# Kernel tuning notes

Hardware: AMD Instinct MI355X
Metric: run time of the kernel (lower is better)

## Reference

```python
import jax, jax.numpy as jnp
import numpy as np

B, C, H, W = 8, 512, 32, 32
NUM_HEADS = 8
HEAD_DIM = C // NUM_HEADS


def setup_inputs() -> dict:
    key = jax.random.key(0)
    k1, k2, k3 = jax.random.split(key, 3)
    query = jax.random.normal(k1, (B, C, H, W), dtype=jnp.float32)
    key_value = jax.random.normal(k2, (B, C, H, W), dtype=jnp.float32)
    # Linear(dim, 3*dim): store as [C, 3C] so y = x @ W + b
    W_qkv = jax.random.normal(k3, (C, 3 * C), dtype=jnp.float32) * (C ** -0.5)
    b_qkv = jnp.zeros((3 * C,), dtype=jnp.float32)
    return {"query": query, "key_value": key_value, "W_qkv": W_qkv, "b_qkv": b_qkv}


def reference(query, key_value, W_qkv, b_qkv):
    Bb, Cc, Hh, Ww = query.shape
    seq = Hh * Ww
    scale = HEAD_DIM ** -0.5

    # [B, C, H, W] -> [B, S, C]
    q_seq = query.reshape(Bb, Cc, seq).transpose(0, 2, 1)
    kv_seq = key_value.reshape(Bb, Cc, seq).transpose(0, 2, 1)

    # Original calls full qkv_proj and slices; math == projecting with sliced weights.
    q = q_seq @ W_qkv[:, :Cc] + b_qkv[:Cc]
    k = kv_seq @ W_qkv[:, Cc:2 * Cc] + b_qkv[Cc:2 * Cc]
    v = kv_seq @ W_qkv[:, 2 * Cc:] + b_qkv[2 * Cc:]

    def heads(x):  # [B, S, C] -> [B, nH, S, hd]
        return x.reshape(Bb, seq, NUM_HEADS, HEAD_DIM).transpose(0, 2, 1, 3)

    q, k, v = heads(q), heads(k), heads(v)
    attn = jnp.einsum('bhqd,bhkd->bhqk', q, k) * scale
    attn = jax.nn.softmax(attn, axis=-1)  # dropout: identity in eval
    out = jnp.einsum('bhqk,bhkd->bhqd', attn, v)
    # [B, nH, S, hd] -> [B, S, C] -> [B, C, H, W]
    out = out.transpose(0, 2, 1, 3).reshape(Bb, seq, Cc)
    return out.transpose(0, 2, 1).reshape(Bb, Cc, Hh, Ww)
```

## Files before the change

kernel.cpp:

```cpp
#include <hip/hip_runtime.h>
#include <hip/hip_bf16.h>

using short4v = __attribute__((ext_vector_type(4))) short;
using short8  = __attribute__((ext_vector_type(8))) short;
using uint2v  = __attribute__((ext_vector_type(2))) unsigned int;
using f32x4   = __attribute__((ext_vector_type(4))) float;

static constexpr int CDIM = 512;
static constexpr float KSCALE = 0.125f * 1.44269504088896341f;

__device__ __forceinline__ short f2bf(float f) {
  unsigned u = __builtin_bit_cast(unsigned, f);
  u = (u + 0x7fffu + ((u >> 16) & 1u)) >> 16;
  return (short)(unsigned short)u;
}
__device__ __forceinline__ unsigned pack_bf16(float a, float b) {
  return (unsigned)(unsigned short)f2bf(a) | ((unsigned)(unsigned short)f2bf(b) << 16);
}

#define GLOAD_LDS16(gp, lp)                                                              \
  __builtin_amdgcn_global_load_lds((const __attribute__((address_space(1))) void*)(gp),  \
                                   (__attribute__((address_space(3))) void*)(lp), 16, 0, 0)
#define MFMA16(a, b, c) __builtin_amdgcn_mfma_f32_16x16x32_bf16((a), (b), (c), 0, 0, 0)
#define WAIT_LGKM0() __builtin_amdgcn_s_waitcnt(0xc07f)

__global__ __launch_bounds__(256) void prep_transpose(const float* __restrict__ query,
                                                      const float* __restrict__ keyv,
                                                      const float* __restrict__ Wqkv,
                                                      short* __restrict__ Xq_t,
                                                      short* __restrict__ Xkv_t,
                                                      short* __restrict__ W_t) {
  __shared__ float tile[64 * 65];
  const int id = blockIdx.x;
  const float* s; short* d; int R, C, r0, c0;
  if (id < 2048) {
    const int which = id >> 10;
    int rem = id & 1023;
    const int b = rem >> 7; rem &= 127;
    R = 512; C = 1024;
    s = (which ? keyv : query) + (size_t)b * 512 * 1024;
    d = (which ? Xkv_t : Xq_t) + (size_t)b * 512 * 1024;
    r0 = (rem >> 4) * 64; c0 = (rem & 15) * 64;
  } else {
    const int rem = id - 2048;
    R = 512; C = 1536; s = Wqkv; d = W_t;
    r0 = (rem / 24) * 64; c0 = (rem % 24) * 64;
  }
  const int t  = threadIdx.x;
  const int rr = t >> 4;
  const int c4 = (t & 15) * 4;
#pragma unroll
  for (int i = 0; i < 4; ++i) {
    const int r = rr + i * 16;
    f32x4 v = *(const f32x4*)(s + (size_t)(r0 + r) * C + c0 + c4);
#pragma unroll
    for (int j = 0; j < 4; ++j) tile[(c4 + j) * 65 + r] = v[j];
  }
  __syncthreads();
  const int r8 = (t & 7) * 8;
#pragma unroll
  for (int i = 0; i < 2; ++i) {
    const int c = (t >> 3) + i * 32;
    short8 pk;
#pragma unroll
    for (int j = 0; j < 8; ++j) pk[j] = f2bf(tile[c * 65 + r8 + j]);
    *(short8*)(d + (size_t)(c0 + c) * R + r0 + r8) = pk;
  }
}

__global__ __launch_bounds__(256, 3) void qkv_gemm(const short* __restrict__ Xq,
                                                   const short* __restrict__ Xkv,
                                                   const short* __restrict__ Wt,
                                                   const float* __restrict__ bias,
                                                   short* __restrict__ Qg,
                                                   short* __restrict__ Kg,
                                                   short* __restrict__ Vt) {
  __shared__ short Asm[128 * 64];
  __shared__ short Bsm[128 * 64];
  __shared__ short epi[4 * 1152];
  const int n0 = blockIdx.x * 128;
  const int m0 = blockIdx.y * 128;
  const short* A = (n0 < CDIM) ? Xq : Xkv;
  const int t = threadIdx.x;
  const int w = t >> 6, l = t & 63;
  const int wm = w & 1, wn = w >> 1;
  const int lc = l & 15, lr = l >> 4;

  f32x4 acc[4][4];
#pragma unroll
  for (int i = 0; i < 4; ++i)
#pragma unroll
    for (int j = 0; j < 4; ++j) acc[i][j] = (f32x4){0.f, 0.f, 0.f, 0.f};

  for (int kb = 0; kb < 8; ++kb) {
    const int k0 = kb * 64;
#pragma unroll
    for (int i = 0; i < 4; ++i) {
      const int Qi = (w * 4 + i) * 64 + l;
      const int m = Qi >> 3, kq = Qi & 7;
      GLOAD_LDS16(A  + (size_t)(m0 + m) * CDIM + k0 + kq * 8, &Asm[Qi * 8]);
      GLOAD_LDS16(Wt + (size_t)(n0 + m) * CDIM + k0 + kq * 8, &Bsm[Qi * 8]);
    }
    __syncthreads();
#pragma unroll
    for (int kc = 0; kc < 2; ++kc) {
      short8 af[4], bfr[4];
#pragma unroll
      for (int mt = 0; mt < 4; ++mt)
        af[mt] = *(const short8*)(&Asm[(wm * 64 + mt * 16 + lc) * 64 + kc * 32 + lr * 8]);
#pragma unroll
      for (int nt = 0; nt < 4; ++nt)
        bfr[nt] = *(const short8*)(&Bsm[(wn * 64 + nt * 16 + lc) * 64 + kc * 32 + lr * 8]);
#pragma unroll
      for (int mt = 0; mt < 4; ++mt)
#pragma unroll
        for (int nt = 0; nt < 4; ++nt)
          acc[mt][nt] = MFMA16(af[mt], bfr[nt], acc[mt][nt]);
    }
    __syncthreads();
  }

  const int N0 = n0 + wn * 64, M0 = m0 + wm * 64;
  const int hg = N0 >> 6;
  const int part = hg >> 3, hh = hg & 7;
  const int bb = M0 >> 10, s0 = M0 & 1023;
  float bv[4];
#pragma unroll
  for (int nt = 0; nt < 4; ++nt) bv[nt] = bias[N0 + nt * 16 + lc];
  short* slab = epi + w * 1152;

  if (part < 2) {
    const float osc = part ? 1.f : KSCALE;
    short* obase = (part ? Kg : Qg) + (size_t)(bb * 8 + hh) * 65536 + (size_t)s0 * 64;
#pragma unroll
    for (int mt = 0; mt < 4; ++mt) {
#pragma unroll
      for (int nt = 0; nt < 4; ++nt)
#pragma unroll
        for (int r = 0; r < 4; ++r)
          slab[(lr * 4 + r) * 72 + nt * 16 + lc] = f2bf((acc[mt][nt][r] + bv[nt]) * osc);
      WAIT_LGKM0();
#pragma unroll
      for (int i = 0; i < 2; ++i) {
        const int slot = i * 64 + l;
        const int m_l = slot >> 3, n8 = (slot & 7) * 8;
        short8 vv = *(const short8*)(&slab[m_l * 72 + n8]);
        *(short8*)(obase + (size_t)(mt * 16 + m_l) * 64 + n8) = vv;
      }
      WAIT_LGKM0();
    }
  } else {
    short* vbase = Vt + (size_t)(bb * 8 + hh) * 65536;
#pragma unroll
    for (int nt = 0; nt < 4; ++nt) {
#pragma unroll
      for (int mt = 0; mt < 4; ++mt)
#pragma unroll
        for (int r = 0; r < 4; ++r)
          slab[lc * 72 + mt * 16 + lr * 4 + r] = f2bf(acc[mt][nt][r] + bv[nt]);
      WAIT_LGKM0();
#pragma unroll
      for (int i = 0; i < 2; ++i) {
        const int slot = i * 64 + l;
        const int dloc = slot >> 3, ch = (slot & 7) * 8;
        short8 vv = *(const short8*)(&slab[dloc * 72 + ch]);
        *(short8*)(vbase + (size_t)(nt * 16 + dloc) * 1024 + s0 + ch) = vv;
      }
      WAIT_LGKM0();
    }
  }
}

__global__ __launch_bounds__(256, 2) void flash_attn(const short* __restrict__ Qg,
                                                     const short* __restrict__ Kg,
                                                     const short* __restrict__ Vt,
                                                     float* __restrict__ out) {
  __shared__ alignas(16) short smem[17408];
  short* Ksm = smem;
  short* Vsm = smem + 4096;
  const int b = blockIdx.z, h = blockIdx.y;
  const int q0 = blockIdx.x * 128;
  const int bh = b * 8 + h;
  const int t = threadIdx.x;
  const int w = t >> 6, l = t & 63;
  const int quad = l >> 4, l15 = l & 15;
  short* Pw = smem + 8192 + w * 2304;

  const short* Qbase = Qg + (size_t)bh * 65536;
  const short* Kbase = Kg + (size_t)bh * 65536;
  const short* Vbase = Vt + (size_t)bh * 65536;

  short8 bq[2][2];
#pragma unroll
  for (int qs = 0; qs < 2; ++qs) {
    const short* qrow = Qbase + (size_t)(q0 + qs * 64 + w * 16 + l15) * 64;
    bq[qs][0] = *(const short8*)(qrow + quad * 8);
    bq[qs][1] = *(const short8*)(qrow + 32 + quad * 8);
  }

  float lp[2] = {0.f, 0.f};
  f32x4 Oac[2][4];
#pragma unroll
  for (int qs = 0; qs < 2; ++qs)
#pragma unroll
    for (int dt = 0; dt < 4; ++dt) Oac[qs][dt] = (f32x4){0.f, 0.f, 0.f, 0.f};

  for (int it = 0; it < 16; ++it) {
    const int kk0 = it * 64;
#pragma unroll
    for (int i = 0; i < 2; ++i) {
      const int Qi = (w * 2 + i) * 64 + l;
      const int sr = Qi >> 3, u = Qi & 7;
      GLOAD_LDS16(Kbase + (size_t)(kk0 + sr) * 64 + (u ^ (sr & 7)) * 8, &Ksm[Qi * 8]);
      GLOAD_LDS16(Vbase + (size_t)sr * 1024 + kk0 + (u ^ (sr & 7)) * 8, &Vsm[Qi * 8]);
    }
    __syncthreads();

    short8 kf[2][4];
#pragma unroll
    for (int c = 0; c < 2; ++c)
#pragma unroll
      for (int nt = 0; nt < 4; ++nt) {
        const int srow = nt * 16 + l15;
        kf[c][nt] = *(const short8*)(&Ksm[(srow * 8 + ((c * 4 + quad) ^ (srow & 7))) * 8]);
      }

#pragma unroll
    for (int qs = 0; qs < 2; ++qs) {
      f32x4 st[4];
#pragma unroll
      for (int nt = 0; nt < 4; ++nt) {
        st[nt] = (f32x4){0.f, 0.f, 0.f, 0.f};
#pragma unroll
        for (int c = 0; c < 2; ++c) st[nt] = MFMA16(kf[c][nt], bq[qs][c], st[nt]);
      }
      short* Ps = Pw + qs * 1152;
#pragma unroll
      for (int nt = 0; nt < 4; ++nt) {
        float p0 = __builtin_amdgcn_exp2f(st[nt][0]);
        float p1 = __builtin_amdgcn_exp2f(st[nt][1]);
        float p2 = __builtin_amdgcn_exp2f(st[nt][2]);
        float p3 = __builtin_amdgcn_exp2f(st[nt][3]);
        lp[qs] += (p0 + p1) + (p2 + p3);
        uint2v pk;
        pk[0] = pack_bf16(p0, p1);
        pk[1] = pack_bf16(p2, p3);
        *(uint2v*)(&Ps[l15 * 72 + (nt * 4 + quad) * 4]) = pk;
      }
    }
    WAIT_LGKM0();

#pragma unroll
    for (int c = 0; c < 2; ++c) {
      short8 pb0 = *(const short8*)(&Pw[l15 * 72 + (c * 8 + quad * 2) * 4]);
      short8 pb1 = *(const short8*)(&Pw[1152 + l15 * 72 + (c * 8 + quad * 2) * 4]);
#pragma unroll
      for (int dt = 0; dt < 4; ++dt) {
        const int drow = dt * 16 + l15;
        short8 vf = *(const short8*)(&Vsm[(drow * 8 + ((c * 4 + quad) ^ (drow & 7))) * 8]);
        Oac[0][dt] = MFMA16(vf, pb0, Oac[0][dt]);
        Oac[1][dt] = MFMA16(vf, pb1, Oac[1][dt]);
      }
    }
    __syncthreads();
  }

#pragma unroll
  for (int qs = 0; qs < 2; ++qs) {
    float lv = lp[qs];
    lv += __shfl_xor(lv, 16, 64);
    lv += __shfl_xor(lv, 32, 64);
    const float rinv = 1.f / lv;
    float* ob = out + ((size_t)(b * 512 + h * 64)) * 1024 + q0 + qs * 64 + w * 16 + l15;
#pragma unroll
    for (int dt = 0; dt < 4; ++dt)
#pragma unroll
      for (int r = 0; r < 4; ++r)
        ob[(size_t)(dt * 16 + quad * 4 + r) * 1024] = Oac[qs][dt][r] * rinv;
  }
}

extern "C" void kernel_launch(void* const* d_in, const int* in_sizes, int n_in,
                              void* d_out, int out_size, void* d_ws, size_t ws_size,
                              hipStream_t stream) {
  const float* query = (const float*)d_in[0];
  const float* keyv  = (const float*)d_in[1];
  const float* Wqkv  = (const float*)d_in[2];
  const float* bqkv  = (const float*)d_in[3];
  float* out = (float*)d_out;
  short* ws  = (short*)d_ws;

  short* Xq_t  = ws;
  short* Xkv_t = ws + 4194304;
  short* W_t   = ws + 8388608;
  short* Qg    = ws + 9175040;
  short* Kg    = ws + 13369344;
  short* Vt    = ws + 17563648;

  prep_transpose<<<dim3(2240), 256, 0, stream>>>(query, keyv, Wqkv, Xq_t, Xkv_t, W_t);
  qkv_gemm<<<dim3(12, 64, 1), 256, 0, stream>>>(Xq_t, Xkv_t, W_t, bqkv, Qg, Kg, Vt);
  flash_attn<<<dim3(8, 8, 8), 256, 0, stream>>>(Qg, Kg, Vt, out);
}
```

Measured before the change: 136.9 us.

## Widen QKV GEMM tile to 128x256, swizzle LDS, reorder attention grid

The QKV projection GEMM tile grows from 128x128 to 128x256, giving each wave 4x8 accumulators and more MFMA work per A-fragment load. Both LDS tiles now use an XOR swizzle on 16-byte chunks to avoid bank conflicts on fragment reads. The epilogue loops over two heads per wave. The attention grid is reordered so batch*head is the fastest-varying block index, which changes the schedule and cache locality of K/V reuse. The costs are higher register pressure and occupancy lowered to 2 blocks per CU, and the GEMM grid drops to 384 blocks.

```diff
diff --git a/kernel.cpp b/kernel.cpp
--- a/kernel.cpp
+++ b/kernel.cpp
@@ -68,7 +68,7 @@
   }
 }
 
-__global__ __launch_bounds__(256, 3) void qkv_gemm(const short* __restrict__ Xq,
+__global__ __launch_bounds__(256, 2) void qkv_gemm(const short* __restrict__ Xq,
                                                    const short* __restrict__ Xkv,
                                                    const short* __restrict__ Wt,
                                                    const float* __restrict__ bias,
@@ -76,9 +76,9 @@
                                                    short* __restrict__ Kg,
                                                    short* __restrict__ Vt) {
   __shared__ short Asm[128 * 64];
-  __shared__ short Bsm[128 * 64];
+  __shared__ short Bsm[256 * 64];
   __shared__ short epi[4 * 1152];
-  const int n0 = blockIdx.x * 128;
+  const int n0 = blockIdx.x * 256;
   const int m0 = blockIdx.y * 128;
   const short* A = (n0 < CDIM) ? Xq : Xkv;
   const int t = threadIdx.x;
@@ -86,87 +86,102 @@
   const int wm = w & 1, wn = w >> 1;
   const int lc = l & 15, lr = l >> 4;
 
-  f32x4 acc[4][4];
+  f32x4 acc[4][8];
 #pragma unroll
   for (int i = 0; i < 4; ++i)
 #pragma unroll
-    for (int j = 0; j < 4; ++j) acc[i][j] = (f32x4){0.f, 0.f, 0.f, 0.f};
+    for (int j = 0; j < 8; ++j) acc[i][j] = (f32x4){0.f, 0.f, 0.f, 0.f};
 
   for (int kb = 0; kb < 8; ++kb) {
     const int k0 = kb * 64;
 #pragma unroll
     for (int i = 0; i < 4; ++i) {
       const int Qi = (w * 4 + i) * 64 + l;
-      const int m = Qi >> 3, kq = Qi & 7;
-      GLOAD_LDS16(A  + (size_t)(m0 + m) * CDIM + k0 + kq * 8, &Asm[Qi * 8]);
-      GLOAD_LDS16(Wt + (size_t)(n0 + m) * CDIM + k0 + kq * 8, &Bsm[Qi * 8]);
+      const int row = Qi >> 3, u = Qi & 7;
+      GLOAD_LDS16(A + (size_t)(m0 + row) * CDIM + k0 + ((u ^ (row & 7)) * 8), &Asm[Qi * 8]);
+    }
+#pragma unroll
+    for (int i = 0; i < 8; ++i) {
+      const int Qi = (w * 8 + i) * 64 + l;
+      const int row = Qi >> 3, u = Qi & 7;
+      GLOAD_LDS16(Wt + (size_t)(n0 + row) * CDIM + k0 + ((u ^ (row & 7)) * 8), &Bsm[Qi * 8]);
     }
     __syncthreads();
 #pragma unroll
     for (int kc = 0; kc < 2; ++kc) {
-      short8 af[4], bfr[4];
+      short8 af[4], bfr[8];
+#pragma unroll
+      for (int mt = 0; mt < 4; ++mt) {
+        const int row = wm * 64 + mt * 16 + lc;
+        af[mt] = *(const short8*)(&Asm[(row * 8 + ((kc * 4 + lr) ^ (row & 7))) * 8]);
+      }
+#pragma unroll
+      for (int nt = 0; nt < 8; ++nt) {
+        const int row = wn * 128 + nt * 16 + lc;
+        bfr[nt] = *(const short8*)(&Bsm[(row * 8 + ((kc * 4 + lr) ^ (row & 7))) * 8]);
+      }
 #pragma unroll
       for (int mt = 0; mt < 4; ++mt)
-        af[mt] = *(const short8*)(&Asm[(wm * 64 + mt * 16 + lc) * 64 + kc * 32 + lr * 8]);
-#pragma unroll
-      for (int nt = 0; nt < 4; ++nt)
-        bfr[nt] = *(const short8*)(&Bsm[(wn * 64 + nt * 16 + lc) * 64 + kc * 32 + lr * 8]);
-#pragma unroll
-      for (int mt = 0; mt < 4; ++mt)
-#pragma unroll
-        for (int nt = 0; nt < 4; ++nt)
+#pragma unroll
+        for (int nt = 0; nt < 8; ++nt)
           acc[mt][nt] = MFMA16(af[mt], bfr[nt], acc[mt][nt]);
     }
     __syncthreads();
   }
 
-  const int N0 = n0 + wn * 64, M0 = m0 + wm * 64;
-  const int hg = N0 >> 6;
-  const int part = hg >> 3, hh = hg & 7;
+  const int M0 = m0 + wm * 64;
   const int bb = M0 >> 10, s0 = M0 & 1023;
-  float bv[4];
-#pragma unroll
-  for (int nt = 0; nt < 4; ++nt) bv[nt] = bias[N0 + nt * 16 + lc];
+  const int N0 = n0 + wn * 128;
+  float bv[8];
+#pragma unroll
+  for (int nt = 0; nt < 8; ++nt) bv[nt] = bias[N0 + nt * 16 + lc];
   short* slab = epi + w * 1152;
 
-  if (part < 2) {
-    const float osc = part ? 1.f : KSCALE;
-    short* obase = (part ? Kg : Qg) + (size_t)(bb * 8 + hh) * 65536 + (size_t)s0 * 64;
-#pragma unroll
-    for (int mt = 0; mt < 4; ++mt) {
-#pragma unroll
-      for (int nt = 0; nt < 4; ++nt)
-#pragma unroll
-        for (int r = 0; r < 4; ++r)
-          slab[(lr * 4 + r) * 72 + nt * 16 + lc] = f2bf((acc[mt][nt][r] + bv[nt]) * osc);
-      WAIT_LGKM0();
-#pragma unroll
-      for (int i = 0; i < 2; ++i) {
-        const int slot = i * 64 + l;
-        const int m_l = slot >> 3, n8 = (slot & 7) * 8;
-        short8 vv = *(const short8*)(&slab[m_l * 72 + n8]);
-        *(short8*)(obase + (size_t)(mt * 16 + m_l) * 64 + n8) = vv;
-      }
-      WAIT_LGKM0();
-    }
-  } else {
-    short* vbase = Vt + (size_t)(bb * 8 + hh) * 65536;
-#pragma unroll
-    for (int nt = 0; nt < 4; ++nt) {
-#pragma unroll
-      for (int mt = 0; mt < 4; ++mt)
-#pragma unroll
-        for (int r = 0; r < 4; ++r)
-          slab[lc * 72 + mt * 16 + lr * 4 + r] = f2bf(acc[mt][nt][r] + bv[nt]);
-      WAIT_LGKM0();
-#pragma unroll
-      for (int i = 0; i < 2; ++i) {
-        const int slot = i * 64 + l;
-        const int dloc = slot >> 3, ch = (slot & 7) * 8;
-        short8 vv = *(const short8*)(&slab[dloc * 72 + ch]);
-        *(short8*)(vbase + (size_t)(nt * 16 + dloc) * 1024 + s0 + ch) = vv;
-      }
-      WAIT_LGKM0();
+#pragma unroll
+  for (int hi = 0; hi < 2; ++hi) {
+    const int hg = (N0 >> 6) + hi;
+    const int part = hg >> 3, hh = hg & 7;
+    const int nb = hi * 4;
+    if (part < 2) {
+      const float osc = part ? 1.f : KSCALE;
+      short* obase = (part ? Kg : Qg) + (size_t)(bb * 8 + hh) * 65536 + (size_t)s0 * 64;
+#pragma unroll
+      for (int mt = 0; mt < 4; ++mt) {
+#pragma unroll
+        for (int ntL = 0; ntL < 4; ++ntL)
+#pragma unroll
+          for (int r = 0; r < 4; ++r)
+            slab[(lr * 4 + r) * 72 + ntL * 16 + lc] =
+                f2bf((acc[mt][nb + ntL][r] + bv[nb + ntL]) * osc);
+        WAIT_LGKM0();
+#pragma unroll
+        for (int i = 0; i < 2; ++i) {
+          const int slot = i * 64 + l;
+          const int m_l = slot >> 3, n8 = (slot & 7) * 8;
+          short8 vv = *(const short8*)(&slab[m_l * 72 + n8]);
+          *(short8*)(obase + (size_t)(mt * 16 + m_l) * 64 + n8) = vv;
+        }
+        WAIT_LGKM0();
+      }
+    } else {
+      short* vbase = Vt + (size_t)(bb * 8 + hh) * 65536;
+#pragma unroll
+      for (int ntL = 0; ntL < 4; ++ntL) {
+#pragma unroll
+        for (int mt = 0; mt < 4; ++mt)
+#pragma unroll
+          for (int r = 0; r < 4; ++r)
+            slab[lc * 72 + mt * 16 + lr * 4 + r] = f2bf(acc[mt][nb + ntL][r] + bv[nb + ntL]);
+        WAIT_LGKM0();
+#pragma unroll
+        for (int i = 0; i < 2; ++i) {
+          const int slot = i * 64 + l;
+          const int dloc = slot >> 3, ch = (slot & 7) * 8;
+          short8 vv = *(const short8*)(&slab[dloc * 72 + ch]);
+          *(short8*)(vbase + (size_t)(ntL * 16 + dloc) * 1024 + s0 + ch) = vv;
+        }
+        WAIT_LGKM0();
+      }
     }
   }
 }
@@ -178,9 +193,9 @@
   __shared__ alignas(16) short smem[17408];
   short* Ksm = smem;
   short* Vsm = smem + 4096;
-  const int b = blockIdx.z, h = blockIdx.y;
-  const int q0 = blockIdx.x * 128;
-  const int bh = b * 8 + h;
+  const int bh = blockIdx.x;
+  const int b = bh >> 3, h = bh & 7;
+  const int q0 = blockIdx.y * 128;
   const int t = threadIdx.x;
   const int w = t >> 6, l = t & 63;
   const int quad = l >> 4, l15 = l & 15;
@@ -298,6 +313,6 @@
   short* Vt    = ws + 17563648;
 
   prep_transpose<<<dim3(2240), 256, 0, stream>>>(query, keyv, Wqkv, Xq_t, Xkv_t, W_t);
-  qkv_gemm<<<dim3(12, 64, 1), 256, 0, stream>>>(Xq_t, Xkv_t, W_t, bqkv, Qg, Kg, Vt);
-  flash_attn<<<dim3(8, 8, 8), 256, 0, stream>>>(Qg, Kg, Vt, out);
-}
+  qkv_gemm<<<dim3(6, 64, 1), 256, 0, stream>>>(Xq_t, Xkv_t, W_t, bqkv, Qg, Kg, Vt);
+  flash_attn<<<dim3(64, 8, 1), 256, 0, stream>>>(Qg, Kg, Vt, out);
+}
```

Result: faster. 134.0 us (-2.1%).
